# Performance work log

Measured on AMD Instinct MI355X. Metric: run time of the kernel, lower is better.

## Reference

```python
import jax, jax.numpy as jnp
import numpy as np

N_NODES = 100000
N_EDGES = 1600000
EDGE_FEAT = 16
EDGE_HID = 32
NODE_FEAT = 128


def setup_inputs() -> dict:
    key = jax.random.key(0)
    ks = jax.random.split(key, 10)
    inp = {
        "edge_logits": jax.random.normal(ks[0], (N_EDGES, 1), dtype=jnp.float32),
        "edge_feats": jax.random.normal(ks[1], (N_EDGES, EDGE_FEAT), dtype=jnp.float32),
        "node_feats": jax.random.normal(ks[2], (N_NODES, NODE_FEAT), dtype=jnp.float32),
        "dst": jax.random.randint(ks[3], (N_EDGES,), 0, N_NODES, dtype=jnp.int32),
        # edge_transform Linear(edge_feat -> edge_hid)
        "W_et": jax.random.normal(ks[4], (EDGE_FEAT, EDGE_HID), dtype=jnp.float32) * (1.0 / np.sqrt(EDGE_FEAT)),
        "b_et": jnp.zeros((EDGE_HID,), dtype=jnp.float32),
        # MLP Linear(edge_hid + node_feat -> node_feat)
        "W1": jax.random.normal(ks[5], (EDGE_HID + NODE_FEAT, NODE_FEAT), dtype=jnp.float32) * (1.0 / np.sqrt(EDGE_HID + NODE_FEAT)),
        "b1": jnp.zeros((NODE_FEAT,), dtype=jnp.float32),
        # MLP Linear(node_feat -> node_feat)
        "W2": jax.random.normal(ks[6], (NODE_FEAT, NODE_FEAT), dtype=jnp.float32) * (1.0 / np.sqrt(NODE_FEAT)),
        "b2": jnp.zeros((NODE_FEAT,), dtype=jnp.float32),
    }
    return inp


def reference(edge_logits, edge_feats, node_feats, dst, W_et, b_et, W1, b1, W2, b2):
    # edge_softmax: segment softmax of edge_logits grouped by destination node
    logits = edge_logits[:, 0]                                        # [E]
    seg_max = jax.ops.segment_max(logits, dst, num_segments=N_NODES)  # [N]
    seg_max = jnp.where(jnp.isfinite(seg_max), seg_max, 0.0)          # guard empty segments
    ex = jnp.exp(logits - seg_max[dst])                               # [E]
    denom = jax.ops.segment_sum(ex, dst, num_segments=N_NODES)        # [N]
    denom = jnp.where(denom == 0.0, 1.0, denom)
    alpha = ex / denom[dst]                                           # [E]
    # edge transform (dropout is identity in eval) then weight by attention
    e = alpha[:, None] * (edge_feats @ W_et + b_et)                   # [E, H]
    # scatter-sum aggregation to destination nodes
    c = jax.ops.segment_sum(e, dst, num_segments=N_NODES)             # [N, H]
    context = jax.nn.elu(c)
    h = jnp.concatenate([context, node_feats], axis=1)                # [N, H+F]
    h = jax.nn.relu(h @ W1 + b1)
    return jax.nn.relu(h @ W2 + b2)                                   # [N, F]
```

## Files before the change

### kernel.cpp

```cpp
#include <hip/hip_runtime.h>

#define EF 16
#define EH 32
#define NF 128
#define K1 160
#define HS 168
#define H2S 136

typedef __attribute__((ext_vector_type(8))) short bf16x8;
typedef __attribute__((ext_vector_type(4))) float f32x4;

__device__ __forceinline__ unsigned short f2b(float f) {
  unsigned u = __float_as_uint(f);
  u += 0x7FFFu + ((u >> 16) & 1u);
  return (unsigned short)(u >> 16);
}

__global__ void k_init(unsigned* __restrict__ cnt, int n,
                       const float* __restrict__ W1, const float* __restrict__ W2,
                       unsigned short* __restrict__ w1t, unsigned short* __restrict__ w2t) {
  int i = blockIdx.x * blockDim.x + threadIdx.x;
  if (i < n) cnt[i] = 0u;
  if (i < K1 * NF) {
    int nn = i / K1, k = i % K1;
    w1t[i] = f2b(W1[k * NF + nn]);
  } else if (i < K1 * NF + NF * NF) {
    int j = i - K1 * NF;
    int nn = j / NF, k = j % NF;
    w2t[j] = f2b(W2[k * NF + nn]);
  }
}

__global__ void k_hist(const int* __restrict__ dst, unsigned* __restrict__ cnt,
                       unsigned* __restrict__ rank, int n_edges) {
  int e = blockIdx.x * blockDim.x + threadIdx.x;
  if (e >= n_edges) return;
  rank[e] = atomicAdd(&cnt[dst[e]], 1u);
}

__global__ void k_scan1(const unsigned* __restrict__ cnt, unsigned* __restrict__ offs,
                        unsigned* __restrict__ bsum, int n) {
  __shared__ unsigned ts[256];
  int t = threadIdx.x;
  int base = blockIdx.x * 1024 + t * 4;
  unsigned v[4];
#pragma unroll
  for (int i = 0; i < 4; ++i) { int idx = base + i; v[i] = (idx < n) ? cnt[idx] : 0u; }
  unsigned run = 0;
#pragma unroll
  for (int i = 0; i < 4; ++i) { unsigned x = v[i]; v[i] = run; run += x; }
  ts[t] = run;
  __syncthreads();
  for (int off = 1; off < 256; off <<= 1) {
    unsigned add = (t >= off) ? ts[t - off] : 0u;
    __syncthreads();
    ts[t] += add;
    __syncthreads();
  }
  unsigned texcl = (t > 0) ? ts[t - 1] : 0u;
  if (t == 255) bsum[blockIdx.x] = ts[255];
#pragma unroll
  for (int i = 0; i < 4; ++i) { int idx = base + i; if (idx < n) offs[idx] = v[i] + texcl; }
}

__global__ void k_scan2(unsigned* __restrict__ bsum, int nb) {
  __shared__ unsigned ts[128];
  int t = threadIdx.x;
  ts[t] = (t < nb) ? bsum[t] : 0u;
  __syncthreads();
  for (int off = 1; off < 128; off <<= 1) {
    unsigned add = (t >= off) ? ts[t - off] : 0u;
    __syncthreads();
    ts[t] += add;
    __syncthreads();
  }
  if (t < nb) bsum[t] = (t > 0) ? ts[t - 1] : 0u;
}

__global__ void k_scan3(unsigned* __restrict__ offs, const unsigned* __restrict__ bsum, int n) {
  int base = blockIdx.x * 1024 + threadIdx.x * 4;
  unsigned add = bsum[blockIdx.x];
#pragma unroll
  for (int i = 0; i < 4; ++i) { int idx = base + i; if (idx < n) offs[idx] += add; }
}

__global__ void k_scatter(const int* __restrict__ dst, const unsigned* __restrict__ rank,
                          const float* __restrict__ logits, const unsigned* __restrict__ offs,
                          uint2* __restrict__ evex, int n_edges) {
  int e = blockIdx.x * blockDim.x + threadIdx.x;
  if (e >= n_edges) return;
  int d = dst[e];
  unsigned slot = offs[d] + rank[e];
  uint2 v;
  v.x = (unsigned)e;
  v.y = __float_as_uint(__expf(logits[e]));
  evex[slot] = v;
}

__global__ __launch_bounds__(256) void k_gather(
    const uint2* __restrict__ evex, const float* __restrict__ efeat,
    const unsigned* __restrict__ cnt, const unsigned* __restrict__ offs,
    const float* __restrict__ W_et, const float* __restrict__ b_et,
    unsigned short* __restrict__ ctxb, int n_nodes) {
  int node = (int)((blockIdx.x * blockDim.x + threadIdx.x) >> 6);
  if (node >= n_nodes) return;
  int lane = threadIdx.x & 63;
  int eo = lane >> 4, k = lane & 15;
  unsigned start = offs[node];
  unsigned deg = cnt[node];
  float sexk = 0.0f, dpart = 0.0f;
  for (unsigned i = eo; i < deg; i += 4) {
    uint2 ev = evex[start + i];
    float ex = __uint_as_float(ev.y);
    float f = efeat[(size_t)ev.x * EF + k];
    sexk += ex * f;
    if (k == 0) dpart += ex;
  }
  sexk += __shfl_xor(sexk, 16);
  sexk += __shfl_xor(sexk, 32);
  dpart += __shfl_xor(dpart, 16);
  dpart += __shfl_xor(dpart, 32);
  float denom = __shfl(dpart, 0);
  float inv = (deg > 0) ? 1.0f / denom : 0.0f;
  float S = (deg > 0) ? 1.0f : 0.0f;
  int j = lane & 31;
  float acc = 0.0f;
#pragma unroll
  for (int k2 = 0; k2 < 16; ++k2) acc += __shfl(sexk, k2) * W_et[k2 * EH + j];
  float c = acc * inv + S * b_et[j];
  float ctxv = (c > 0.0f) ? c : (__expf(c) - 1.0f);
  if (lane < 32) ctxb[(size_t)node * EH + lane] = f2b(ctxv);
}

__global__ __launch_bounds__(256) void k_node(
    const unsigned short* __restrict__ ctxb, const float* __restrict__ nf,
    const unsigned short* __restrict__ w1t, const unsigned short* __restrict__ w2t,
    const float* __restrict__ b1, const float* __restrict__ b2,
    float* __restrict__ out, int n_nodes) {
  __shared__ __align__(16) unsigned short hA[64 * HS];
  __shared__ __align__(16) unsigned short hB[64 * H2S];
  const int t = threadIdx.x;
  const int w = t >> 6, lane = t & 63;
  const int m = lane & 15, q = lane >> 4;
  int n0 = blockIdx.x * 64;
  if (n0 + 64 > n_nodes) n0 = n_nodes - 64;

  {
    int node = t >> 2, j = (t & 3) * 8;
    *(uint4*)&hA[node * HS + j] = *(const uint4*)&ctxb[(size_t)(n0 + node) * EH + j];
  }
#pragma unroll
  for (int i = 0; i < 8; ++i) {
    int idx = t + 256 * i;
    int node = idx >> 5, j = (idx & 31) * 4;
    float4 v = *(const float4*)&nf[(size_t)(n0 + node) * NF + j];
    unsigned short r[4] = {f2b(v.x), f2b(v.y), f2b(v.z), f2b(v.w)};
    *(uint2*)&hA[node * HS + EH + j] = *(const uint2*)r;
  }
  __syncthreads();

  const int mr = w * 16;
  f32x4 acc[8];
#pragma unroll
  for (int nt = 0; nt < 8; ++nt) acc[nt] = (f32x4){0.f, 0.f, 0.f, 0.f};
  for (int ks = 0; ks < 5; ++ks) {
    bf16x8 a = *(const bf16x8*)&hA[(mr + m) * HS + ks * 32 + q * 8];
#pragma unroll
    for (int nt = 0; nt < 8; ++nt) {
      bf16x8 b = *(const bf16x8*)&w1t[(size_t)(nt * 16 + m) * K1 + ks * 32 + q * 8];
      acc[nt] = __builtin_amdgcn_mfma_f32_16x16x32_bf16(a, b, acc[nt], 0, 0, 0);
    }
  }
#pragma unroll
  for (int nt = 0; nt < 8; ++nt) {
    float bb = b1[nt * 16 + m];
#pragma unroll
    for (int r = 0; r < 4; ++r) {
      float v = fmaxf(acc[nt][r] + bb, 0.0f);
      hB[(mr + q * 4 + r) * H2S + nt * 16 + m] = f2b(v);
    }
  }
  __syncthreads();

  f32x4 ac2[8];
#pragma unroll
  for (int nt = 0; nt < 8; ++nt) ac2[nt] = (f32x4){0.f, 0.f, 0.f, 0.f};
  for (int ks = 0; ks < 4; ++ks) {
    bf16x8 a = *(const bf16x8*)&hB[(mr + m) * H2S + ks * 32 + q * 8];
#pragma unroll
    for (int nt = 0; nt < 8; ++nt) {
      bf16x8 b = *(const bf16x8*)&w2t[(size_t)(nt * 16 + m) * NF + ks * 32 + q * 8];
      ac2[nt] = __builtin_amdgcn_mfma_f32_16x16x32_bf16(a, b, ac2[nt], 0, 0, 0);
    }
  }
#pragma unroll
  for (int nt = 0; nt < 8; ++nt) {
    float bb = b2[nt * 16 + m];
#pragma unroll
    for (int r = 0; r < 4; ++r) {
      out[(size_t)(n0 + mr + q * 4 + r) * NF + nt * 16 + m] = fmaxf(ac2[nt][r] + bb, 0.0f);
    }
  }
}

extern "C" void kernel_launch(void* const* d_in, const int* in_sizes, int n_in,
                              void* d_out, int out_size, void* d_ws, size_t ws_size,
                              hipStream_t stream) {
  const float* edge_logits = (const float*)d_in[0];
  const float* edge_feats  = (const float*)d_in[1];
  const float* node_feats  = (const float*)d_in[2];
  const int*   dst         = (const int*)d_in[3];
  const float* W_et        = (const float*)d_in[4];
  const float* b_et        = (const float*)d_in[5];
  const float* W1          = (const float*)d_in[6];
  const float* b1          = (const float*)d_in[7];
  const float* W2          = (const float*)d_in[8];
  const float* b2          = (const float*)d_in[9];
  float* out = (float*)d_out;

  const int E = in_sizes[0];
  const int n = in_sizes[2] / NF;

  unsigned* cnt  = (unsigned*)d_ws;
  unsigned* offs = cnt + n;
  unsigned* bsum = offs + n;
  unsigned* rank = bsum + 128;
  uint2*    evex = (uint2*)(rank + E);
  unsigned short* ctxb = (unsigned short*)(evex + E);
  unsigned short* w1t  = ctxb + (size_t)n * EH;
  unsigned short* w2t  = w1t + NF * K1;

  const int thr = 256;
  const int nscan = (n + 1023) / 1024;

  k_init<<<(n + thr - 1) / thr, thr, 0, stream>>>(cnt, n, W1, W2, w1t, w2t);
  k_hist<<<(E + thr - 1) / thr, thr, 0, stream>>>(dst, cnt, rank, E);
  k_scan1<<<nscan, 256, 0, stream>>>(cnt, offs, bsum, n);
  k_scan2<<<1, 128, 0, stream>>>(bsum, nscan);
  k_scan3<<<nscan, 256, 0, stream>>>(offs, bsum, n);
  k_scatter<<<(E + thr - 1) / thr, thr, 0, stream>>>(dst, rank, edge_logits, offs, evex, E);
  k_gather<<<(n * 64 + thr - 1) / thr, thr, 0, stream>>>(evex, edge_feats, cnt, offs,
                                                         W_et, b_et, ctxb, n);
  k_node<<<(n + 63) / 64, 256, 0, stream>>>(ctxb, node_feats, w1t, w2t, b1, b2, out, n);
}
```

Baseline: 438.7 us.

## Scatter pre-weighted bf16 edge features into CSR order and merge scan kernels

The scatter kernel now reads each edge's features coalesced in original order, multiplies them by exp(logit), packs them to bf16 and writes them contiguously in destination-sorted order, along with a separate exp array. The gather kernel then streams contiguous rows instead of doing random reads of edge features through an index. This trades a random gather for a random scatter write and rounds the products to bf16 before summation, which lowers precision. The two scan finishing kernels are merged into one: each block redoes the block-sum scan in shared memory, which removes one launch.

```diff
diff --git a/kernel.cpp b/kernel.cpp
--- a/kernel.cpp
+++ b/kernel.cpp
@@ -14,6 +14,9 @@
   unsigned u = __float_as_uint(f);
   u += 0x7FFFu + ((u >> 16) & 1u);
   return (unsigned short)(u >> 16);
+}
+__device__ __forceinline__ unsigned pack2b(float a, float b) {
+  return (unsigned)f2b(a) | ((unsigned)f2b(b) << 16);
 }
 
 __global__ void k_init(unsigned* __restrict__ cnt, int n,
@@ -63,72 +66,89 @@
   for (int i = 0; i < 4; ++i) { int idx = base + i; if (idx < n) offs[idx] = v[i] + texcl; }
 }
 
-__global__ void k_scan2(unsigned* __restrict__ bsum, int nb) {
-  __shared__ unsigned ts[128];
+__global__ void k_scan3(unsigned* __restrict__ offs, const unsigned* __restrict__ bsum,
+                        int n, int nb) {
+  __shared__ unsigned ts[256];
   int t = threadIdx.x;
   ts[t] = (t < nb) ? bsum[t] : 0u;
   __syncthreads();
-  for (int off = 1; off < 128; off <<= 1) {
+  for (int off = 1; off < 256; off <<= 1) {
     unsigned add = (t >= off) ? ts[t - off] : 0u;
     __syncthreads();
     ts[t] += add;
     __syncthreads();
   }
-  if (t < nb) bsum[t] = (t > 0) ? ts[t - 1] : 0u;
-}
-
-__global__ void k_scan3(unsigned* __restrict__ offs, const unsigned* __restrict__ bsum, int n) {
-  int base = blockIdx.x * 1024 + threadIdx.x * 4;
-  unsigned add = bsum[blockIdx.x];
+  unsigned add = (blockIdx.x > 0) ? ts[blockIdx.x - 1] : 0u;
+  int base = blockIdx.x * 1024 + t * 4;
 #pragma unroll
   for (int i = 0; i < 4; ++i) { int idx = base + i; if (idx < n) offs[idx] += add; }
 }
 
 __global__ void k_scatter(const int* __restrict__ dst, const unsigned* __restrict__ rank,
                           const float* __restrict__ logits, const unsigned* __restrict__ offs,
-                          uint2* __restrict__ evex, int n_edges) {
+                          const float* __restrict__ efeat,
+                          unsigned* __restrict__ prodb, float* __restrict__ exs, int n_edges) {
   int e = blockIdx.x * blockDim.x + threadIdx.x;
   if (e >= n_edges) return;
   int d = dst[e];
   unsigned slot = offs[d] + rank[e];
-  uint2 v;
-  v.x = (unsigned)e;
-  v.y = __float_as_uint(__expf(logits[e]));
-  evex[slot] = v;
+  float ex = __expf(logits[e]);
+  exs[slot] = ex;
+  const float4* fp = (const float4*)(efeat + (size_t)e * EF);
+  float4 v0 = fp[0], v1 = fp[1], v2 = fp[2], v3 = fp[3];
+  uint4 o0, o1;
+  o0.x = pack2b(ex * v0.x, ex * v0.y);
+  o0.y = pack2b(ex * v0.z, ex * v0.w);
+  o0.z = pack2b(ex * v1.x, ex * v1.y);
+  o0.w = pack2b(ex * v1.z, ex * v1.w);
+  o1.x = pack2b(ex * v2.x, ex * v2.y);
+  o1.y = pack2b(ex * v2.z, ex * v2.w);
+  o1.z = pack2b(ex * v3.x, ex * v3.y);
+  o1.w = pack2b(ex * v3.z, ex * v3.w);
+  uint4* pp = (uint4*)(prodb + (size_t)slot * 8);
+  pp[0] = o0;
+  pp[1] = o1;
 }
 
 __global__ __launch_bounds__(256) void k_gather(
-    const uint2* __restrict__ evex, const float* __restrict__ efeat,
+    const unsigned* __restrict__ prodb, const float* __restrict__ exs,
     const unsigned* __restrict__ cnt, const unsigned* __restrict__ offs,
     const float* __restrict__ W_et, const float* __restrict__ b_et,
     unsigned short* __restrict__ ctxb, int n_nodes) {
   int node = (int)((blockIdx.x * blockDim.x + threadIdx.x) >> 6);
   if (node >= n_nodes) return;
   int lane = threadIdx.x & 63;
-  int eo = lane >> 4, k = lane & 15;
   unsigned start = offs[node];
   unsigned deg = cnt[node];
-  float sexk = 0.0f, dpart = 0.0f;
-  for (unsigned i = eo; i < deg; i += 4) {
-    uint2 ev = evex[start + i];
-    float ex = __uint_as_float(ev.y);
-    float f = efeat[(size_t)ev.x * EF + k];
-    sexk += ex * f;
-    if (k == 0) dpart += ex;
-  }
-  sexk += __shfl_xor(sexk, 16);
-  sexk += __shfl_xor(sexk, 32);
-  dpart += __shfl_xor(dpart, 16);
-  dpart += __shfl_xor(dpart, 32);
-  float denom = __shfl(dpart, 0);
-  float inv = (deg > 0) ? 1.0f / denom : 0.0f;
+  int rg = lane >> 3, c = lane & 7;
+  float a0 = 0.0f, a1 = 0.0f;
+  for (unsigned i = rg; i < deg; i += 8) {
+    unsigned p = prodb[(size_t)(start + i) * 8 + c];
+    a0 += __uint_as_float(p << 16);
+    a1 += __uint_as_float(p & 0xFFFF0000u);
+  }
+  a0 += __shfl_xor(a0, 8);  a1 += __shfl_xor(a1, 8);
+  a0 += __shfl_xor(a0, 16); a1 += __shfl_xor(a1, 16);
+  a0 += __shfl_xor(a0, 32); a1 += __shfl_xor(a1, 32);
+  float dsum = 0.0f;
+  for (unsigned i = lane; i < deg; i += 64) dsum += exs[start + i];
+  dsum += __shfl_xor(dsum, 1);
+  dsum += __shfl_xor(dsum, 2);
+  dsum += __shfl_xor(dsum, 4);
+  dsum += __shfl_xor(dsum, 8);
+  dsum += __shfl_xor(dsum, 16);
+  dsum += __shfl_xor(dsum, 32);
+  float inv = (deg > 0) ? 1.0f / dsum : 0.0f;
   float S = (deg > 0) ? 1.0f : 0.0f;
   int j = lane & 31;
   float acc = 0.0f;
 #pragma unroll
-  for (int k2 = 0; k2 < 16; ++k2) acc += __shfl(sexk, k2) * W_et[k2 * EH + j];
-  float c = acc * inv + S * b_et[j];
-  float ctxv = (c > 0.0f) ? c : (__expf(c) - 1.0f);
+  for (int k = 0; k < 16; ++k) {
+    float sk = (k & 1) ? __shfl(a1, k >> 1) : __shfl(a0, k >> 1);
+    acc += sk * W_et[k * EH + j];
+  }
+  float cv = acc * inv + S * b_et[j];
+  float ctxv = (cv > 0.0f) ? cv : (__expf(cv) - 1.0f);
   if (lane < 32) ctxb[(size_t)node * EH + lane] = f2b(ctxv);
 }
 
@@ -221,12 +241,13 @@
   const int E = in_sizes[0];
   const int n = in_sizes[2] / NF;
 
-  unsigned* cnt  = (unsigned*)d_ws;
-  unsigned* offs = cnt + n;
-  unsigned* bsum = offs + n;
-  unsigned* rank = bsum + 128;
-  uint2*    evex = (uint2*)(rank + E);
-  unsigned short* ctxb = (unsigned short*)(evex + E);
+  unsigned* cnt   = (unsigned*)d_ws;
+  unsigned* offs  = cnt + n;
+  unsigned* bsum  = offs + n;
+  unsigned* rank  = bsum + 256;
+  float*    exs   = (float*)(rank + E);
+  unsigned* prodb = (unsigned*)(exs + E);
+  unsigned short* ctxb = (unsigned short*)(prodb + (size_t)E * 8);
   unsigned short* w1t  = ctxb + (size_t)n * EH;
   unsigned short* w2t  = w1t + NF * K1;
 
@@ -236,10 +257,10 @@
   k_init<<<(n + thr - 1) / thr, thr, 0, stream>>>(cnt, n, W1, W2, w1t, w2t);
   k_hist<<<(E + thr - 1) / thr, thr, 0, stream>>>(dst, cnt, rank, E);
   k_scan1<<<nscan, 256, 0, stream>>>(cnt, offs, bsum, n);
-  k_scan2<<<1, 128, 0, stream>>>(bsum, nscan);
-  k_scan3<<<nscan, 256, 0, stream>>>(offs, bsum, n);
-  k_scatter<<<(E + thr - 1) / thr, thr, 0, stream>>>(dst, rank, edge_logits, offs, evex, E);
-  k_gather<<<(n * 64 + thr - 1) / thr, thr, 0, stream>>>(evex, edge_feats, cnt, offs,
+  k_scan3<<<nscan, 256, 0, stream>>>(offs, bsum, n, nscan);
+  k_scatter<<<(E + thr - 1) / thr, thr, 0, stream>>>(dst, rank, edge_logits, offs, edge_feats,
+                                                     prodb, exs, E);
+  k_gather<<<(n * 64 + thr - 1) / thr, thr, 0, stream>>>(prodb, exs, cnt, offs,
                                                          W_et, b_et, ctxb, n);
   k_node<<<(n + 63) / 64, 256, 0, stream>>>(ctxb, node_feats, w1t, w2t, b1, b2, out, n);
 }
```

Measured after the change: 429.8 us. 2.0% less time.
